# Kernel optimization log

Hardware: AMD Instinct MI355X
Metric: run time of the kernel (lower is better)

Reference implementation:

```python
import jax, jax.numpy as jnp
import numpy as np

B, S, E, H, DH = 256, 256, 384, 6, 64
NEG_INF = -1e9


def setup_inputs() -> dict:
    key = jax.random.key(0)
    ks = jax.random.split(key, 8)
    sc = 0.02
    return {
        "x": jax.random.normal(ks[0], (B, S, E), jnp.float32),
        "Wq": jax.random.normal(ks[1], (H, E, DH), jnp.float32) * sc,
        "Wk": jax.random.normal(ks[2], (H, E, DH), jnp.float32) * sc,
        "Wv": jax.random.normal(ks[3], (H, E, DH), jnp.float32) * sc,
        "Wp": jax.random.normal(ks[4], (E, E), jnp.float32) * sc,
        "bp": jnp.zeros((E,), jnp.float32),
        "W1": jax.random.normal(ks[5], (E, 4 * E), jnp.float32) * sc,
        "b1": jnp.zeros((4 * E,), jnp.float32),
        "W2": jax.random.normal(ks[6], (4 * E, E), jnp.float32) * sc,
        "b2": jnp.zeros((E,), jnp.float32),
        "g1": jnp.ones((E,), jnp.float32),
        "be1": jnp.zeros((E,), jnp.float32),
        "g2": jnp.ones((E,), jnp.float32),
        "be2": jnp.zeros((E,), jnp.float32),
    }


def _layernorm(x, g, b, eps=1e-5):
    mu = jnp.mean(x, axis=-1, keepdims=True)
    var = jnp.mean(jnp.square(x - mu), axis=-1, keepdims=True)
    return (x - mu) * jax.lax.rsqrt(var + eps) * g + b


def reference(x, Wq, Wk, Wv, Wp, bp, W1, b1, W2, b2, g1, be1, g2, be2):
    # --- pre-attention LayerNorm ---
    h = _layernorm(x, g1, be1)
    # --- multi-head causal self-attention (all heads vectorized) ---
    q = jnp.einsum('bse,hed->bhsd', h, Wq)
    k = jnp.einsum('bse,hed->bhsd', h, Wk)
    v = jnp.einsum('bse,hed->bhsd', h, Wv)
    scores = jnp.einsum('bhsd,bhtd->bhst', q, k) * (DH ** -0.5)
    causal = jnp.tril(jnp.ones((S, S), dtype=bool))
    scores = jnp.where(causal, scores, NEG_INF)
    att = jax.nn.softmax(scores, axis=-1)  # dropout = identity at eval
    o = jnp.einsum('bhst,bhtd->bhsd', att, v)
    o = o.transpose(0, 2, 1, 3).reshape(x.shape[0], S, E)  # concat heads
    x = x + (o @ Wp + bp)
    # --- FFN block ---
    h2 = _layernorm(x, g2, be2)
    ffn = jax.nn.relu(h2 @ W1 + b1) @ W2 + b2
    return x + ffn
```

## Files before the change

### kernel.cpp

```cpp
#include <hip/hip_runtime.h>
#include <hip/hip_bf16.h>
#include <stdint.h>

typedef __bf16 bf16_t;
typedef __bf16 bf16x2 __attribute__((ext_vector_type(2)));
typedef __bf16 bf16x8 __attribute__((ext_vector_type(8)));
typedef float f32x4 __attribute__((ext_vector_type(4)));

#define NB 256
#define NS 256
#define NE 384
#define NH 6
#define ND 64
#define NM (NB*NS)

__device__ __forceinline__ f32x4 mfma16(bf16x8 a, bf16x8 b, f32x4 c) {
    return __builtin_amdgcn_mfma_f32_16x16x32_bf16(a, b, c, 0, 0, 0);
}

__device__ __forceinline__ void cp16_async(const bf16_t* g, const bf16_t* l) {
    __builtin_amdgcn_global_load_lds(
        (__attribute__((address_space(1))) void*)g,
        (__attribute__((address_space(3))) void*)l, 16, 0, 0);
}

__global__ void wqkv_trans(const float* __restrict__ Wq, const float* __restrict__ Wk,
                           const float* __restrict__ Wv, bf16_t* __restrict__ Wcat)
{
    int i = blockIdx.x * 256 + threadIdx.x;
    if (i >= NH*NE*ND) return;
    int d = i & 63;
    int e = (i >> 6) % NE;
    int h = i / (NE*ND);
    int n = h*64 + d;
    Wcat[(size_t)(0*NE*NH*ND) + (size_t)n*NE + e]            = (bf16_t)Wq[i];
    Wcat[(size_t)(NE)*(NH*ND) + (size_t)(384 + n)*NE + e - (size_t)(NE)*(NH*ND)] = (bf16_t)Wk[i];
    Wcat[(size_t)(768 + n)*NE + e]                            = (bf16_t)Wv[i];
}

__global__ void wtrans(const float* __restrict__ src, bf16_t* __restrict__ dst, int K, int N)
{
    int i = blockIdx.x * 256 + threadIdx.x;
    if (i >= K*N) return;
    int k = i / N, n = i % N;
    dst[(size_t)n*K + k] = (bf16_t)src[i];
}

__global__ __launch_bounds__(256) void ln_kernel(
    const float* __restrict__ x, const float* __restrict__ g,
    const float* __restrict__ be, bf16_t* __restrict__ o)
{
    const int wave = threadIdx.x >> 6, lane = threadIdx.x & 63;
    const int row = blockIdx.x * 4 + wave;
    const float* xr = x + (size_t)row * NE;
    float v[6]; float s = 0.f, sq = 0.f;
    #pragma unroll
    for (int i = 0; i < 6; i++) { v[i] = xr[i*64 + lane]; s += v[i]; sq += v[i]*v[i]; }
    #pragma unroll
    for (int off = 32; off > 0; off >>= 1) { s += __shfl_xor(s, off); sq += __shfl_xor(sq, off); }
    const float mean = s * (1.f/NE);
    const float rstd = rsqrtf(sq * (1.f/NE) - mean*mean + 1e-5f);
    bf16_t* orow = o + (size_t)row * NE;
    #pragma unroll
    for (int i = 0; i < 6; i++) {
        int e = i*64 + lane;
        orow[e] = (bf16_t)((v[i] - mean) * rstd * g[e] + be[e]);
    }
}

template<int OUT_MODE, bool RELU>
__global__ __launch_bounds__(512, 2) void gemm_wide(
    const bf16_t* __restrict__ A, const bf16_t* __restrict__ Bt,
    void* __restrict__ outp, const float* __restrict__ bias,
    const float* __restrict__ res, int M, int N, int K, int ldb)
{
    __shared__ bf16_t sAB[3][512*32];
    const int tid = threadIdx.x;
    const int wave = tid >> 6, lane = tid & 63;
    const int l15 = lane & 15, quad = lane >> 4;
    const int m0 = blockIdx.x * 128;
    const int n0 = blockIdx.y * 384;
    const int wm = wave >> 2, wn = wave & 3;

    const int srow = lane >> 2;
    const int scol = (lane & 3) * 8;
    const int r0 = 64 * wave;

    const bf16_t* gsrc;
    size_t rs;
    if (wave < 2) { gsrc = A  + (size_t)(m0 + r0 + srow) * K + scol;              rs = (size_t)K; }
    else          { gsrc = Bt + (size_t)(n0 + r0 - 128 + srow) * ldb + scol;      rs = (size_t)ldb; }

    const f32x4 zero = {0.f, 0.f, 0.f, 0.f};
    f32x4 acc[4][6];
    #pragma unroll
    for (int a = 0; a < 4; a++)
        #pragma unroll
        for (int b = 0; b < 6; b++) acc[a][b] = zero;

    const int nk = K >> 5;

    auto issue = [&](int t, int slot) {
        const int kt = t << 5;
        #pragma unroll
        for (int i = 0; i < 4; i++)
            cp16_async(gsrc + (size_t)(16*i)*rs + kt, &sAB[slot][(r0 + 16*i)*32]);
    };

    issue(0, 0);
    issue(1, 1);

    int cb = 0;
    int ns = 2;
    for (int it = 0; it < nk; ++it) {
        asm volatile("s_barrier" ::: "memory");
        if (it + 2 < nk) {
            issue(it + 2, ns);
            asm volatile("s_waitcnt vmcnt(8)\n\ts_barrier" ::: "memory");
        } else if (it + 1 < nk) {
            asm volatile("s_waitcnt vmcnt(4)\n\ts_barrier" ::: "memory");
        } else {
            asm volatile("s_waitcnt vmcnt(0)\n\ts_barrier" ::: "memory");
        }

        bf16x8 bfr[6];
        #pragma unroll
        for (int i = 0; i < 6; i++)
            bfr[i] = *(const bf16x8*)&sAB[cb][(128 + 96*wn + 16*i + l15)*32 + quad*8];
        #pragma unroll
        for (int mi = 0; mi < 4; mi++) {
            bf16x8 af = *(const bf16x8*)&sAB[cb][(64*wm + 16*mi + l15)*32 + quad*8];
            #pragma unroll
            for (int ni = 0; ni < 6; ni++)
                acc[mi][ni] = mfma16(af, bfr[ni], acc[mi][ni]);
        }

        cb = (cb == 2) ? 0 : cb + 1;
        ns = (ns == 2) ? 0 : ns + 1;
    }

    #pragma unroll
    for (int mi = 0; mi < 4; mi++) {
        #pragma unroll
        for (int ni = 0; ni < 6; ni++) {
            #pragma unroll
            for (int r = 0; r < 4; r++) {
                int gm = m0 + 64*wm + 16*mi + quad*4 + r;
                int gn = n0 + 96*wn + 16*ni + l15;
                float v = acc[mi][ni][r];
                if (bias) v += bias[gn];
                if (res)  v += res[(size_t)gm*N + gn];
                if (RELU) v = fmaxf(v, 0.f);
                if (OUT_MODE == 1) {
                    int sel = (gn >= 768) ? 2 : ((gn >= 384) ? 1 : 0);
                    int within = gn - sel*384;
                    int b = gm >> 8, s = gm & 255, h = within >> 6, d = within & 63;
                    ((bf16_t*)outp)[(size_t)sel*((size_t)NM*384) +
                                    (((size_t)b*NH + h)*NS + s)*ND + d] = (bf16_t)v;
                } else if (OUT_MODE == 2) {
                    ((float*)outp)[(size_t)gm*N + gn] = v;
                } else {
                    ((bf16_t*)outp)[(size_t)gm*N + gn] = (bf16_t)v;
                }
            }
        }
    }
}

__global__ __launch_bounds__(256) void attn_kernel(
    const bf16_t* __restrict__ Qg, const bf16_t* __restrict__ Kg,
    const bf16_t* __restrict__ Vg, bf16_t* __restrict__ Og)
{
    __shared__ bf16_t sK[256*72];
    __shared__ bf16_t sVT[64*264];
    __shared__ bf16_t sQ[64*72];
    __shared__ bf16_t sS[64*264];
    __shared__ float sMax[64*4];
    __shared__ float sSum[64*4];
    __shared__ float sRowSum[64];

    const int tid = threadIdx.x;
    const int wave = tid >> 6, lane = tid & 63;
    const int l15 = lane & 15, quad = lane >> 4;
    const int bh = blockIdx.x;
    const int b = bh / NH, h = bh % NH;
    const size_t base = (size_t)bh * (NS*ND);
    const bf16_t* Qb = Qg + base;
    const bf16_t* Kb = Kg + base;
    const bf16_t* Vb = Vg + base;

    #pragma unroll
    for (int it = 0; it < 8; it++) {
        int idx = it*256 + tid;
        int t = idx >> 3, c = idx & 7;
        bf16x8 kv = *(const bf16x8*)(Kb + t*64 + c*8);
        *(bf16x8*)&sK[t*72 + c*8] = kv;
        bf16x8 vv = *(const bf16x8*)(Vb + t*64 + c*8);
        #pragma unroll
        for (int j = 0; j < 8; j++) sVT[(c*8 + j)*264 + t] = vv[j];
    }

    const int r = lane;
    const int p = wave;
    const f32x4 zero = {0.f, 0.f, 0.f, 0.f};

    for (int mt = 0; mt < 4; mt++) {
        __syncthreads();
        #pragma unroll
        for (int it = 0; it < 2; it++) {
            int idx = it*256 + tid;
            int qr = idx >> 3, c = idx & 7;
            *(bf16x8*)&sQ[qr*72 + c*8] = *(const bf16x8*)(Qb + (64*mt + qr)*64 + c*8);
        }
        __syncthreads();
        if (wave <= mt) {
            const int ct = wave;
            bf16x8 bk[2][4];
            #pragma unroll
            for (int ks = 0; ks < 2; ks++)
                #pragma unroll
                for (int ni = 0; ni < 4; ni++)
                    bk[ks][ni] = *(const bf16x8*)&sK[(64*ct + 16*ni + l15)*72 + ks*32 + quad*8];
            #pragma unroll
            for (int mi = 0; mi < 4; mi++) {
                bf16x8 a0 = *(const bf16x8*)&sQ[(16*mi + l15)*72 + quad*8];
                bf16x8 a1 = *(const bf16x8*)&sQ[(16*mi + l15)*72 + 32 + quad*8];
                f32x4 sc[4];
                #pragma unroll
                for (int ni = 0; ni < 4; ni++) sc[ni] = zero;
                #pragma unroll
                for (int ni = 0; ni < 4; ni++) sc[ni] = mfma16(a0, bk[0][ni], sc[ni]);
                #pragma unroll
                for (int ni = 0; ni < 4; ni++) sc[ni] = mfma16(a1, bk[1][ni], sc[ni]);
                #pragma unroll
                for (int ni = 0; ni < 4; ni++)
                    #pragma unroll
                    for (int rr = 0; rr < 4; rr++)
                        sS[(16*mi + quad*4 + rr)*264 + 64*ct + 16*ni + l15] =
                            (bf16_t)(sc[ni][rr] * 0.125f);
            }
        }
        __syncthreads();
        const int sg = 64*mt + r;
        float mx = -INFINITY;
        if (p <= mt) {
            #pragma unroll
            for (int c = 0; c < 8; c++) {
                bf16x8 v8 = *(const bf16x8*)&sS[r*264 + 64*p + c*8];
                #pragma unroll
                for (int j = 0; j < 8; j++) {
                    int t = 64*p + c*8 + j;
                    float v = (float)v8[j];
                    mx = (t <= sg) ? fmaxf(mx, v) : mx;
                }
            }
        }
        sMax[r*4 + p] = mx;
        __syncthreads();
        const float rmax = fmaxf(fmaxf(sMax[r*4+0], sMax[r*4+1]),
                                 fmaxf(sMax[r*4+2], sMax[r*4+3]));
        float sum = 0.f;
        if (p <= mt) {
            #pragma unroll
            for (int c = 0; c < 8; c++) {
                bf16x8 v8 = *(const bf16x8*)&sS[r*264 + 64*p + c*8];
                bf16x8 e8;
                #pragma unroll
                for (int j = 0; j < 8; j++) {
                    int t = 64*p + c*8 + j;
                    float e = 0.f;
                    if (t <= sg) e = __expf((float)v8[j] - rmax);
                    sum += e;
                    e8[j] = (bf16_t)e;
                }
                *(bf16x8*)&sS[r*264 + 64*p + c*8] = e8;
            }
        }
        sSum[r*4 + p] = sum;
        __syncthreads();
        if (p == 0) sRowSum[r] = sSum[r*4+0] + sSum[r*4+1] + sSum[r*4+2] + sSum[r*4+3];
        __syncthreads();
        f32x4 oacc[4];
        #pragma unroll
        for (int ni = 0; ni < 4; ni++) oacc[ni] = zero;
        for (int kt = 0; kt <= mt; kt++) {
            bf16x8 a = *(const bf16x8*)&sS[(16*p + l15)*264 + 64*kt + quad*8];
            #pragma unroll
            for (int ni = 0; ni < 4; ni++) {
                bf16x8 bv = *(const bf16x8*)&sVT[(16*ni + l15)*264 + 64*kt + quad*8];
                oacc[ni] = mfma16(a, bv, oacc[ni]);
            }
        }
        #pragma unroll
        for (int ni = 0; ni < 4; ni++) {
            #pragma unroll
            for (int rr = 0; rr < 4; rr++) {
                int lrow = 16*p + quad*4 + rr;
                float inv = 1.0f / sRowSum[lrow];
                int srow_g = 64*mt + lrow;
                int d = 16*ni + l15;
                Og[((size_t)(b*NS + srow_g))*NE + h*ND + d] = (bf16_t)(oacc[ni][rr] * inv);
            }
        }
    }
}

extern "C" void kernel_launch(void* const* d_in, const int* in_sizes, int n_in,
                              void* d_out, int out_size, void* d_ws, size_t ws_size,
                              hipStream_t stream)
{
    (void)in_sizes; (void)n_in; (void)out_size; (void)ws_size;
    const float* x   = (const float*)d_in[0];
    const float* Wq  = (const float*)d_in[1];
    const float* Wk  = (const float*)d_in[2];
    const float* Wv  = (const float*)d_in[3];
    const float* Wp  = (const float*)d_in[4];
    const float* bp  = (const float*)d_in[5];
    const float* W1  = (const float*)d_in[6];
    const float* b1  = (const float*)d_in[7];
    const float* W2  = (const float*)d_in[8];
    const float* b2  = (const float*)d_in[9];
    const float* g1  = (const float*)d_in[10];
    const float* be1 = (const float*)d_in[11];
    const float* g2  = (const float*)d_in[12];
    const float* be2 = (const float*)d_in[13];
    float* out = (float*)d_out;

    char* ws = (char*)d_ws;
    const size_t SZ = (size_t)NM * NE * 2;
    bf16_t* h_bf  = (bf16_t*)(ws);
    bf16_t* q_bf  = (bf16_t*)(ws + SZ);
    bf16_t* k_bf  = (bf16_t*)(ws + 2*SZ);
    bf16_t* v_bf  = (bf16_t*)(ws + 3*SZ);
    bf16_t* o_bf  = (bf16_t*)(ws);
    bf16_t* h2_bf = (bf16_t*)(ws);
    bf16_t* hid   = (bf16_t*)(ws + SZ);
    char* wb = ws + 4*SZ;
    bf16_t* Wcat = (bf16_t*)(wb);
    bf16_t* Wpt  = (bf16_t*)(wb + 884736);
    bf16_t* W1t  = (bf16_t*)(wb + 884736 + 294912);
    bf16_t* W2t  = (bf16_t*)(wb + 884736 + 294912 + 1179648);

    wqkv_trans<<<(NH*NE*ND + 255)/256, 256, 0, stream>>>(Wq, Wk, Wv, Wcat);
    wtrans<<<(NE*NE + 255)/256, 256, 0, stream>>>(Wp, Wpt, NE, NE);
    wtrans<<<(NE*4*NE + 255)/256, 256, 0, stream>>>(W1, W1t, NE, 4*NE);
    wtrans<<<(NE*4*NE + 255)/256, 256, 0, stream>>>(W2, W2t, 4*NE, NE);

    ln_kernel<<<NM/4, 256, 0, stream>>>(x, g1, be1, h_bf);

    dim3 gqkv(NM/128, 3), g1col(NM/128, 1), g2col(NM/128, 2);
    gemm_wide<1,false><<<gqkv, 512, 0, stream>>>(h_bf, Wcat, q_bf, nullptr, nullptr, NM, 1152, NE, NE);

    attn_kernel<<<NB*NH, 256, 0, stream>>>(q_bf, k_bf, v_bf, o_bf);

    gemm_wide<2,false><<<g1col, 512, 0, stream>>>(o_bf, Wpt, out, bp, x, NM, NE, NE, NE);

    ln_kernel<<<NM/4, 256, 0, stream>>>(out, g2, be2, h2_bf);

    gemm_wide<3,true ><<<g2col, 512, 0, stream>>>(h2_bf, W1t, hid, b1, nullptr, NM, 768, NE, NE);
    gemm_wide<2,false><<<g1col, 512, 0, stream>>>(hid, W2t, out, b2, out, NM, NE, 768, 1536);

    gemm_wide<3,true ><<<g2col, 512, 0, stream>>>(h2_bf, W1t + (size_t)768*NE, hid, b1 + 768, nullptr, NM, 768, NE, NE);
    gemm_wide<2,false><<<g1col, 512, 0, stream>>>(hid, W2t + 768, out, nullptr, out, NM, NE, 768, 1536);
}
```

Baseline: 1.061 ms.

## Add persistent weight-stationary GEMM for K=384 projections and restructure FFN split

Result: slower. 1.331 ms (+25.4%).

```diff
diff --git a/kernel.cpp b/kernel.cpp
--- a/kernel.cpp
+++ b/kernel.cpp
@@ -33,9 +33,9 @@
     int e = (i >> 6) % NE;
     int h = i / (NE*ND);
     int n = h*64 + d;
-    Wcat[(size_t)(0*NE*NH*ND) + (size_t)n*NE + e]            = (bf16_t)Wq[i];
-    Wcat[(size_t)(NE)*(NH*ND) + (size_t)(384 + n)*NE + e - (size_t)(NE)*(NH*ND)] = (bf16_t)Wk[i];
-    Wcat[(size_t)(768 + n)*NE + e]                            = (bf16_t)Wv[i];
+    Wcat[(size_t)n*NE + e]         = (bf16_t)Wq[i];
+    Wcat[(size_t)(384 + n)*NE + e] = (bf16_t)Wk[i];
+    Wcat[(size_t)(768 + n)*NE + e] = (bf16_t)Wv[i];
 }
 
 __global__ void wtrans(const float* __restrict__ src, bf16_t* __restrict__ dst, int K, int N)
@@ -65,6 +65,100 @@
     for (int i = 0; i < 6; i++) {
         int e = i*64 + lane;
         orow[e] = (bf16_t)((v[i] - mean) * rstd * g[e] + be[e]);
+    }
+}
+
+template<int OUT_MODE, bool RELU>
+__global__ __launch_bounds__(512, 2) void gemm_persist(
+    const bf16_t* __restrict__ A, const bf16_t* __restrict__ Bt,
+    void* __restrict__ outp, const float* __restrict__ bias,
+    const float* __restrict__ res, int M, int N)
+{
+    __shared__ bf16_t sW[12*192*32];
+
+    const int tid = threadIdx.x;
+    const int wv = tid >> 6, lane = tid & 63;
+    const int l15 = lane & 15, quad = lane >> 4;
+    const int qs = quad ^ (l15 & 3);
+    const int n0 = blockIdx.y * 192;
+
+    #pragma unroll
+    for (int i = 0; i < 18; i++) {
+        int idx = i*512 + tid;
+        int row = idx / 48;
+        int q48 = idx % 48;
+        int kc = q48 >> 2, q = q48 & 3;
+        bf16x8 v = *(const bf16x8*)(Bt + (size_t)(n0 + row)*NE + kc*32 + q*8);
+        *(bf16x8*)&sW[(kc*192 + row)*32 + (q ^ (row & 3))*8] = v;
+    }
+    __syncthreads();
+
+    float bias_v[12];
+    #pragma unroll
+    for (int ni = 0; ni < 12; ni++)
+        bias_v[ni] = bias ? bias[n0 + ni*16 + l15] : 0.f;
+
+    const bf16_t* Ap = A + (size_t)(wv*16 + l15)*NE + quad*8;
+    const int nstrips = M >> 7;
+
+    bf16x8 aA[12], aB[12];
+
+    auto loadA = [&](bf16x8* dst, int s) {
+        const bf16_t* p = Ap + (size_t)s*128*NE;
+        #pragma unroll
+        for (int kc = 0; kc < 12; kc++) dst[kc] = *(const bf16x8*)(p + kc*32);
+    };
+
+    auto computeStore = [&](const bf16x8* a, int s) {
+        const int rowb = s*128 + wv*16;
+        #pragma unroll
+        for (int ng = 0; ng < 3; ng++) {
+            f32x4 acc[4];
+            const f32x4 zero = {0.f, 0.f, 0.f, 0.f};
+            #pragma unroll
+            for (int j = 0; j < 4; j++) acc[j] = zero;
+            #pragma unroll
+            for (int kc = 0; kc < 12; kc++) {
+                #pragma unroll
+                for (int j = 0; j < 4; j++) {
+                    const int r = (ng*4 + j)*16 + l15;
+                    bf16x8 bfrag = *(const bf16x8*)&sW[(kc*192 + r)*32 + qs*8];
+                    acc[j] = mfma16(a[kc], bfrag, acc[j]);
+                }
+            }
+            #pragma unroll
+            for (int j = 0; j < 4; j++) {
+                const int ni = ng*4 + j;
+                const int gn = n0 + ni*16 + l15;
+                #pragma unroll
+                for (int rr = 0; rr < 4; rr++) {
+                    const int gm = rowb + quad*4 + rr;
+                    float v = acc[j][rr] + bias_v[ni];
+                    if (res) v += res[(size_t)gm*N + gn];
+                    if (RELU) v = fmaxf(v, 0.f);
+                    if (OUT_MODE == 1) {
+                        int sel = (gn >= 768) ? 2 : ((gn >= 384) ? 1 : 0);
+                        int within = gn - sel*384;
+                        int b = gm >> 8, s2 = gm & 255, h = within >> 6, d = within & 63;
+                        ((bf16_t*)outp)[(size_t)sel*((size_t)NM*384) +
+                                        (((size_t)b*NH + h)*NS + s2)*ND + d] = (bf16_t)v;
+                    } else if (OUT_MODE == 2) {
+                        ((float*)outp)[(size_t)gm*N + gn] = v;
+                    } else {
+                        ((bf16_t*)outp)[(size_t)gm*N + gn] = (bf16_t)v;
+                    }
+                }
+            }
+        }
+    };
+
+    const int g = gridDim.x;
+    loadA(aA, blockIdx.x);
+    for (int s = blockIdx.x; s < nstrips; s += 2*g) {
+        loadA(aB, s + g);
+        computeStore(aA, s);
+        if (s + 2*g < nstrips) loadA(aA, s + 2*g);
+        computeStore(aB, s + g);
     }
 }
 
@@ -88,8 +182,8 @@
 
     const bf16_t* gsrc;
     size_t rs;
-    if (wave < 2) { gsrc = A  + (size_t)(m0 + r0 + srow) * K + scol;              rs = (size_t)K; }
-    else          { gsrc = Bt + (size_t)(n0 + r0 - 128 + srow) * ldb + scol;      rs = (size_t)ldb; }
+    if (wave < 2) { gsrc = A  + (size_t)(m0 + r0 + srow) * K + scol;         rs = (size_t)K; }
+    else          { gsrc = Bt + (size_t)(n0 + r0 - 128 + srow) * ldb + scol; rs = (size_t)ldb; }
 
     const f32x4 zero = {0.f, 0.f, 0.f, 0.f};
     f32x4 acc[4][6];
@@ -151,13 +245,7 @@
                 if (bias) v += bias[gn];
                 if (res)  v += res[(size_t)gm*N + gn];
                 if (RELU) v = fmaxf(v, 0.f);
-                if (OUT_MODE == 1) {
-                    int sel = (gn >= 768) ? 2 : ((gn >= 384) ? 1 : 0);
-                    int within = gn - sel*384;
-                    int b = gm >> 8, s = gm & 255, h = within >> 6, d = within & 63;
-                    ((bf16_t*)outp)[(size_t)sel*((size_t)NM*384) +
-                                    (((size_t)b*NH + h)*NS + s)*ND + d] = (bf16_t)v;
-                } else if (OUT_MODE == 2) {
+                if (OUT_MODE == 2) {
                     ((float*)outp)[(size_t)gm*N + gn] = v;
                 } else {
                     ((bf16_t*)outp)[(size_t)gm*N + gn] = (bf16_t)v;
@@ -348,18 +436,23 @@
 
     ln_kernel<<<NM/4, 256, 0, stream>>>(x, g1, be1, h_bf);
 
-    dim3 gqkv(NM/128, 3), g1col(NM/128, 1), g2col(NM/128, 2);
-    gemm_wide<1,false><<<gqkv, 512, 0, stream>>>(h_bf, Wcat, q_bf, nullptr, nullptr, NM, 1152, NE, NE);
+    gemm_persist<1,false><<<dim3(128, 6), 512, 0, stream>>>(
+        h_bf, Wcat, q_bf, nullptr, nullptr, NM, 1152);
 
     attn_kernel<<<NB*NH, 256, 0, stream>>>(q_bf, k_bf, v_bf, o_bf);
 
-    gemm_wide<2,false><<<g1col, 512, 0, stream>>>(o_bf, Wpt, out, bp, x, NM, NE, NE, NE);
+    gemm_persist<2,false><<<dim3(128, 2), 512, 0, stream>>>(
+        o_bf, Wpt, out, bp, x, NM, NE);
 
     ln_kernel<<<NM/4, 256, 0, stream>>>(out, g2, be2, h2_bf);
 
-    gemm_wide<3,true ><<<g2col, 512, 0, stream>>>(h2_bf, W1t, hid, b1, nullptr, NM, 768, NE, NE);
-    gemm_wide<2,false><<<g1col, 512, 0, stream>>>(hid, W2t, out, b2, out, NM, NE, 768, 1536);
-
-    gemm_wide<3,true ><<<g2col, 512, 0, stream>>>(h2_bf, W1t + (size_t)768*NE, hid, b1 + 768, nullptr, NM, 768, NE, NE);
-    gemm_wide<2,false><<<g1col, 512, 0, stream>>>(hid, W2t + 768, out, nullptr, out, NM, NE, 768, 1536);
-}
+    for (int half = 0; half < 2; half++) {
+        const size_t roff = (size_t)half * 32768;
+        const bf16_t* h2h = h2_bf + roff * NE;
+        float* outh = out + roff * NE;
+        gemm_persist<3,true><<<dim3(128, 8), 512, 0, stream>>>(
+            h2h, W1t, hid, b1, nullptr, 32768, 1536);
+        gemm_wide<2,false><<<dim3(256, 1), 512, 0, stream>>>(
+            hid, W2t, outh, b2, outh, 32768, NE, 1536, 1536);
+    }
+}
```

## Keep A rows in registers and stream swizzled weight tiles through LDS

Applied to the files above, without the earlier changes.

Measured after the change: 878.1 us. -17.2%, faster.

```diff
diff --git a/kernel.cpp b/kernel.cpp
--- a/kernel.cpp
+++ b/kernel.cpp
@@ -33,9 +33,9 @@
     int e = (i >> 6) % NE;
     int h = i / (NE*ND);
     int n = h*64 + d;
-    Wcat[(size_t)(0*NE*NH*ND) + (size_t)n*NE + e]            = (bf16_t)Wq[i];
-    Wcat[(size_t)(NE)*(NH*ND) + (size_t)(384 + n)*NE + e - (size_t)(NE)*(NH*ND)] = (bf16_t)Wk[i];
-    Wcat[(size_t)(768 + n)*NE + e]                            = (bf16_t)Wv[i];
+    Wcat[(size_t)n*NE + e]         = (bf16_t)Wq[i];
+    Wcat[(size_t)(384 + n)*NE + e] = (bf16_t)Wk[i];
+    Wcat[(size_t)(768 + n)*NE + e] = (bf16_t)Wv[i];
 }
 
 __global__ void wtrans(const float* __restrict__ src, bf16_t* __restrict__ dst, int K, int N)
@@ -69,100 +69,161 @@
 }
 
 template<int OUT_MODE, bool RELU>
-__global__ __launch_bounds__(512, 2) void gemm_wide(
-    const bf16_t* __restrict__ A, const bf16_t* __restrict__ Bt,
+__global__ __launch_bounds__(512, 1) void gemm_areg(
+    const bf16_t* __restrict__ A, int lda,
+    const bf16_t* __restrict__ Bt, int ldb,
     void* __restrict__ outp, const float* __restrict__ bias,
-    const float* __restrict__ res, int M, int N, int K, int ldb)
-{
-    __shared__ bf16_t sAB[3][512*32];
+    const float* __restrict__ res, int N)
+{
+    __shared__ bf16_t sW[3][24576];
     const int tid = threadIdx.x;
-    const int wave = tid >> 6, lane = tid & 63;
+    const int wv = tid >> 6, lane = tid & 63;
     const int l15 = lane & 15, quad = lane >> 4;
     const int m0 = blockIdx.x * 128;
-    const int n0 = blockIdx.y * 384;
-    const int wm = wave >> 2, wn = wave & 3;
-
-    const int srow = lane >> 2;
-    const int scol = (lane & 3) * 8;
-    const int r0 = 64 * wave;
-
-    const bf16_t* gsrc;
-    size_t rs;
-    if (wave < 2) { gsrc = A  + (size_t)(m0 + r0 + srow) * K + scol;              rs = (size_t)K; }
-    else          { gsrc = Bt + (size_t)(n0 + r0 - 128 + srow) * ldb + scol;      rs = (size_t)ldb; }
-
-    const f32x4 zero = {0.f, 0.f, 0.f, 0.f};
-    f32x4 acc[4][6];
-    #pragma unroll
-    for (int a = 0; a < 4; a++)
-        #pragma unroll
-        for (int b = 0; b < 6; b++) acc[a][b] = zero;
-
-    const int nk = K >> 5;
-
-    auto issue = [&](int t, int slot) {
-        const int kt = t << 5;
-        #pragma unroll
-        for (int i = 0; i < 4; i++)
-            cp16_async(gsrc + (size_t)(16*i)*rs + kt, &sAB[slot][(r0 + 16*i)*32]);
+    const int nc = N >> 6;
+
+    uint32_t bo[6];
+    #pragma unroll
+    for (int i = 0; i < 6; i++) {
+        int idx = i*512 + tid;
+        int row = idx / 48, sp = idx % 48;
+        bo[i] = (uint32_t)(row * (ldb*2)) + (((uint32_t)(sp*16)) ^ ((uint32_t)((row & 7) << 4)));
+    }
+    const char* Bbase = (const char*)Bt;
+
+    auto issue = [&](int c, int slot) {
+        const char* src = Bbase + (size_t)c * ((size_t)64 * ldb * 2);
+        bf16_t* dstb = (bf16_t*)((char*)&sW[slot][0] + tid*16);
+        #pragma unroll
+        for (int i = 0; i < 6; i++)
+            cp16_async((const bf16_t*)(src + bo[i]), dstb + i*4096);
     };
+
+    const int arow = m0 + wv*16 + l15;
+    bf16x8 a[12];
+    #pragma unroll
+    for (int kc = 0; kc < 12; kc++)
+        a[kc] = *(const bf16x8*)(A + (size_t)arow*lda + kc*32 + quad*8);
 
     issue(0, 0);
     issue(1, 1);
 
-    int cb = 0;
-    int ns = 2;
-    for (int it = 0; it < nk; ++it) {
+    const int swz = (l15 & 7) << 4;
+    int cb = 0, ns = 2;
+    for (int j = 0; j < nc; ++j) {
         asm volatile("s_barrier" ::: "memory");
-        if (it + 2 < nk) {
-            issue(it + 2, ns);
-            asm volatile("s_waitcnt vmcnt(8)\n\ts_barrier" ::: "memory");
-        } else if (it + 1 < nk) {
-            asm volatile("s_waitcnt vmcnt(4)\n\ts_barrier" ::: "memory");
-        } else {
-            asm volatile("s_waitcnt vmcnt(0)\n\ts_barrier" ::: "memory");
-        }
-
-        bf16x8 bfr[6];
-        #pragma unroll
-        for (int i = 0; i < 6; i++)
-            bfr[i] = *(const bf16x8*)&sAB[cb][(128 + 96*wn + 16*i + l15)*32 + quad*8];
-        #pragma unroll
-        for (int mi = 0; mi < 4; mi++) {
-            bf16x8 af = *(const bf16x8*)&sAB[cb][(64*wm + 16*mi + l15)*32 + quad*8];
-            #pragma unroll
-            for (int ni = 0; ni < 6; ni++)
-                acc[mi][ni] = mfma16(af, bfr[ni], acc[mi][ni]);
-        }
-
-        cb = (cb == 2) ? 0 : cb + 1;
-        ns = (ns == 2) ? 0 : ns + 1;
-    }
-
-    #pragma unroll
-    for (int mi = 0; mi < 4; mi++) {
-        #pragma unroll
-        for (int ni = 0; ni < 6; ni++) {
-            #pragma unroll
-            for (int r = 0; r < 4; r++) {
-                int gm = m0 + 64*wm + 16*mi + quad*4 + r;
-                int gn = n0 + 96*wn + 16*ni + l15;
-                float v = acc[mi][ni][r];
-                if (bias) v += bias[gn];
+        if (j + 2 < nc) issue(j + 2, ns);
+        asm volatile("s_waitcnt vmcnt(12)\n\ts_barrier" ::: "memory");
+
+        #pragma unroll
+        for (int ni = 0; ni < 4; ni++) {
+            f32x4 acc = {0.f, 0.f, 0.f, 0.f};
+            const int rowoff = (ni*16 + l15) * 768;
+            #pragma unroll
+            for (int kc = 0; kc < 12; kc++) {
+                const int kb = (kc*64 + quad*16) ^ swz;
+                bf16x8 wf = *(const bf16x8*)((const char*)&sW[cb][0] + rowoff + kb);
+                acc = mfma16(a[kc], wf, acc);
+            }
+            const int gn = j*64 + ni*16 + l15;
+            const float bv = bias ? bias[gn] : 0.f;
+            #pragma unroll
+            for (int rr = 0; rr < 4; rr++) {
+                const int gm = m0 + wv*16 + quad*4 + rr;
+                float v = acc[rr] + bv;
                 if (res)  v += res[(size_t)gm*N + gn];
                 if (RELU) v = fmaxf(v, 0.f);
                 if (OUT_MODE == 1) {
                     int sel = (gn >= 768) ? 2 : ((gn >= 384) ? 1 : 0);
                     int within = gn - sel*384;
-                    int b = gm >> 8, s = gm & 255, h = within >> 6, d = within & 63;
+                    int b = gm >> 8, s2 = gm & 255, h = within >> 6, d = within & 63;
                     ((bf16_t*)outp)[(size_t)sel*((size_t)NM*384) +
-                                    (((size_t)b*NH + h)*NS + s)*ND + d] = (bf16_t)v;
+                                    (((size_t)b*NH + h)*NS + s2)*ND + d] = (bf16_t)v;
                 } else if (OUT_MODE == 2) {
                     ((float*)outp)[(size_t)gm*N + gn] = v;
                 } else {
                     ((bf16_t*)outp)[(size_t)gm*N + gn] = (bf16_t)v;
                 }
             }
+        }
+        cb = (cb == 2) ? 0 : cb + 1;
+        ns = (ns == 2) ? 0 : ns + 1;
+    }
+}
+
+__global__ __launch_bounds__(512, 1) void gemm_ffn2(
+    const bf16_t* __restrict__ hid,
+    const bf16_t* __restrict__ W2t,
+    float* __restrict__ outp,
+    const float* __restrict__ b2)
+{
+    __shared__ bf16_t sW[3][24576];
+    const int tid = threadIdx.x;
+    const int wv = tid >> 6, lane = tid & 63;
+    const int l15 = lane & 15, quad = lane >> 4;
+    const int m0 = blockIdx.x * 128;
+
+    uint32_t bo[6];
+    #pragma unroll
+    for (int i = 0; i < 6; i++) {
+        int idx = i*512 + tid;
+        int row = idx >> 3, sp = idx & 7;
+        bo[i] = (uint32_t)(row * 3072) + (((uint32_t)(sp*16)) ^ ((uint32_t)((row & 7) << 4)));
+    }
+
+    auto issue = [&](int c, int slot) {
+        const char* src = (const char*)W2t + c*128;
+        bf16_t* dstb = (bf16_t*)((char*)&sW[slot][0] + tid*16);
+        #pragma unroll
+        for (int i = 0; i < 6; i++)
+            cp16_async((const bf16_t*)(src + bo[i]), dstb + i*4096);
+    };
+
+    const bf16_t* Ap = hid + (size_t)(m0 + wv*16 + l15)*1536 + quad*8;
+
+    f32x4 acc[24];
+    #pragma unroll
+    for (int i = 0; i < 24; i++) acc[i] = (f32x4){0.f, 0.f, 0.f, 0.f};
+
+    issue(0, 0);
+    issue(1, 1);
+
+    bf16x8 aC0 = *(const bf16x8*)(Ap);
+    bf16x8 aC1 = *(const bf16x8*)(Ap + 32);
+    bf16x8 aN0, aN1;
+
+    const int swz = (l15 & 7) << 4;
+    int cb = 0, ns = 2;
+    for (int j = 0; j < 24; ++j) {
+        asm volatile("s_barrier" ::: "memory");
+        if (j + 2 < 24) issue(j + 2, ns);
+        asm volatile("s_waitcnt vmcnt(12)\n\ts_barrier" ::: "memory");
+        if (j + 1 < 24) {
+            aN0 = *(const bf16x8*)(Ap + (j+1)*64);
+            aN1 = *(const bf16x8*)(Ap + (j+1)*64 + 32);
+        }
+        #pragma unroll
+        for (int ni = 0; ni < 24; ni++) {
+            const int rowoff = (ni*16 + l15) * 128;
+            bf16x8 w0 = *(const bf16x8*)((const char*)&sW[cb][0] + rowoff + ((quad*16) ^ swz));
+            bf16x8 w1 = *(const bf16x8*)((const char*)&sW[cb][0] + rowoff + ((64 + quad*16) ^ swz));
+            acc[ni] = mfma16(aC0, w0, acc[ni]);
+            acc[ni] = mfma16(aC1, w1, acc[ni]);
+        }
+        aC0 = aN0; aC1 = aN1;
+        cb = (cb == 2) ? 0 : cb + 1;
+        ns = (ns == 2) ? 0 : ns + 1;
+    }
+
+    #pragma unroll
+    for (int ni = 0; ni < 24; ni++) {
+        const int gn = ni*16 + l15;
+        const float bv = b2[gn];
+        #pragma unroll
+        for (int rr = 0; rr < 4; rr++) {
+            const int gm = m0 + wv*16 + quad*4 + rr;
+            float* p = outp + (size_t)gm*384 + gn;
+            *p = *p + acc[ni][rr] + bv;
         }
     }
 }
@@ -348,18 +409,22 @@
 
     ln_kernel<<<NM/4, 256, 0, stream>>>(x, g1, be1, h_bf);
 
-    dim3 gqkv(NM/128, 3), g1col(NM/128, 1), g2col(NM/128, 2);
-    gemm_wide<1,false><<<gqkv, 512, 0, stream>>>(h_bf, Wcat, q_bf, nullptr, nullptr, NM, 1152, NE, NE);
+    gemm_areg<1,false><<<NM/128, 512, 0, stream>>>(
+        h_bf, NE, Wcat, NE, q_bf, nullptr, nullptr, 1152);
 
     attn_kernel<<<NB*NH, 256, 0, stream>>>(q_bf, k_bf, v_bf, o_bf);
 
-    gemm_wide<2,false><<<g1col, 512, 0, stream>>>(o_bf, Wpt, out, bp, x, NM, NE, NE, NE);
+    gemm_areg<2,false><<<NM/128, 512, 0, stream>>>(
+        o_bf, NE, Wpt, NE, out, bp, x, NE);
 
     ln_kernel<<<NM/4, 256, 0, stream>>>(out, g2, be2, h2_bf);
 
-    gemm_wide<3,true ><<<g2col, 512, 0, stream>>>(h2_bf, W1t, hid, b1, nullptr, NM, 768, NE, NE);
-    gemm_wide<2,false><<<g1col, 512, 0, stream>>>(hid, W2t, out, b2, out, NM, NE, 768, 1536);
-
-    gemm_wide<3,true ><<<g2col, 512, 0, stream>>>(h2_bf, W1t + (size_t)768*NE, hid, b1 + 768, nullptr, NM, 768, NE, NE);
-    gemm_wide<2,false><<<g1col, 512, 0, stream>>>(hid, W2t + 768, out, nullptr, out, NM, NE, 768, 1536);
-}
+    for (int half = 0; half < 2; half++) {
+        const size_t roff = (size_t)half * 32768;
+        const bf16_t* h2h = h2_bf + roff * NE;
+        float* outh = out + roff * NE;
+        gemm_areg<3,true><<<32768/128, 512, 0, stream>>>(
+            h2h, NE, W1t, NE, hid, b1, nullptr, 1536);
+        gemm_ffn2<<<32768/128, 512, 0, stream>>>(hid, W2t, outh, b2);
+    }
+}
```
